# Performance work log

Measured on AMD Instinct MI355X. Metric: run time of the kernel, lower is better.

## Reference

```python
import jax, jax.numpy as jnp
import numpy as np

D_MODEL = 1024
N_HEADS = 16
D_HEAD = D_MODEL // N_HEADS


def setup_inputs() -> dict:
    key = jax.random.key(0)
    k1, k2, k3 = jax.random.split(key, 3)
    B, T = 4, 2048
    x = jax.random.normal(k1, (B, T, D_MODEL), dtype=jnp.float32)
    # torch Linear(d, 3d, bias=False): y = x @ W.T ; we store W already transposed -> [d, 3d]
    w_qkv = jax.random.normal(k2, (D_MODEL, 3 * D_MODEL), dtype=jnp.float32) * (D_MODEL ** -0.5)
    w_proj = jax.random.normal(k3, (D_MODEL, D_MODEL), dtype=jnp.float32) * (D_MODEL ** -0.5)
    return {"x": x, "w_qkv": w_qkv, "w_proj": w_proj}


def reference(x, w_qkv, w_proj):
    B, T, C = x.shape
    H, Dh = N_HEADS, D_HEAD
    qkv = (x @ w_qkv).reshape(B, T, 3, H, Dh)
    q = jnp.transpose(qkv[:, :, 0], (0, 2, 1, 3))  # [B,H,T,Dh]
    k = jnp.transpose(qkv[:, :, 1], (0, 2, 1, 3))
    v = jnp.transpose(qkv[:, :, 2], (0, 2, 1, 3))
    scale = 1.0 / jnp.sqrt(jnp.asarray(Dh, dtype=x.dtype))
    att = jnp.einsum('bhqd,bhkd->bhqk', q, k) * scale  # [B,H,T,T]
    causal = jnp.tril(jnp.ones((T, T), dtype=bool))
    att = jnp.where(causal[None, None], att, jnp.asarray(-jnp.inf, dtype=att.dtype))
    att = jax.nn.softmax(att, axis=-1)
    y = jnp.einsum('bhqk,bhkd->bhqd', att, v)          # [B,H,T,Dh]
    y = jnp.transpose(y, (0, 2, 1, 3)).reshape(B, T, C)
    return y @ w_proj
```

## Files before the change

### kernel.cpp

```cpp
#include <hip/hip_runtime.h>
#include <hip/hip_bf16.h>
#include <cmath>

#define T_SEQ 2048
#define NHEADS 16
#define DHEAD 64
#define DMODEL 1024
#define CQKV 3072

typedef __attribute__((ext_vector_type(8))) short short8;
typedef __attribute__((ext_vector_type(8))) __bf16 bf16x8;
typedef __attribute__((ext_vector_type(4))) float floatx4;

#define LDS_CAST(p) ((__attribute__((address_space(3))) void*)(p))
#define GLB_CAST(p) ((const __attribute__((address_space(1))) void*)(p))

static __device__ __forceinline__ floatx4 mfma_bf16(short8 a, short8 b, floatx4 c) {
  return __builtin_amdgcn_mfma_f32_16x16x32_bf16(
      __builtin_bit_cast(bf16x8, a), __builtin_bit_cast(bf16x8, b), c, 0, 0, 0);
}

static __device__ __forceinline__ short f2bf(float f) {
  union { float f; unsigned u; } x; x.f = f;
  unsigned r = x.u + 0x7FFFu + ((x.u >> 16) & 1u);
  return (short)(r >> 16);
}

static __device__ __forceinline__ float bf2f(short s) {
  return __builtin_bit_cast(float, ((unsigned)(unsigned short)s) << 16);
}

static __device__ __forceinline__ float exp2_(float x) {
#if __has_builtin(__builtin_amdgcn_exp2f)
  return __builtin_amdgcn_exp2f(x);
#else
  return exp2f(x);
#endif
}

static __device__ __forceinline__ bool sniff_is_bf16(const unsigned* __restrict__ x) {
  int cnt = 0;
#pragma unroll
  for (int i = 0; i < 32; ++i) {
    unsigned e = (x[i] >> 7) & 0xFFu;
    cnt += (e >= 0x70u && e <= 0x8Fu) ? 1 : 0;
  }
  return cnt >= 16;
}

static __device__ __forceinline__ short8 load8f32(const char* p, size_t idx) {
  const float4* f = (const float4*)(p + idx * 4);
  float4 a = f[0], b = f[1];
  short8 r;
  r[0] = f2bf(a.x); r[1] = f2bf(a.y); r[2] = f2bf(a.z); r[3] = f2bf(a.w);
  r[4] = f2bf(b.x); r[5] = f2bf(b.y); r[6] = f2bf(b.z); r[7] = f2bf(b.w);
  return r;
}

__global__ __launch_bounds__(256) void prep(const char* __restrict__ x,
                                            short* __restrict__ xbf,
                                            const char* __restrict__ wqkv,
                                            short* __restrict__ wqkvT,
                                            const char* __restrict__ wproj,
                                            short* __restrict__ wprojT,
                                            const unsigned* __restrict__ xs) {
  const bool isbf = sniff_is_bf16(xs);
  const int bid = blockIdx.x;
  if (bid < 4096) {
    const int i = (bid * 256 + threadIdx.x) * 8;
    if (isbf) *(short8*)(xbf + i) = *(const short8*)((const short*)x + i);
    else      *(short8*)(xbf + i) = load8f32(x, (size_t)i);
    return;
  }
  __shared__ short tile[32][33];
  const char* w; short* wt; int N, bid2;
  if (bid < 4096 + 3072) { w = wqkv;  wt = wqkvT;  N = 3072; bid2 = bid - 4096; }
  else                   { w = wproj; wt = wprojT; N = 1024; bid2 = bid - 7168; }
  const int K = 1024;
  const int ntiles = N >> 5;
  const int n0 = (bid2 % ntiles) * 32, k0 = (bid2 / ntiles) * 32;
  const int tx = threadIdx.x & 31, ty = threadIdx.x >> 5;
#pragma unroll
  for (int i = 0; i < 4; ++i) {
    const int r = ty * 4 + i;
    const size_t off = (size_t)(k0 + r) * N + n0 + tx;
    tile[r][tx] = isbf ? ((const short*)w)[off] : f2bf(((const float*)w)[off]);
  }
  __syncthreads();
#pragma unroll
  for (int i = 0; i < 4; ++i) {
    const int r = ty * 4 + i;
    wt[(size_t)(n0 + r) * K + k0 + tx] = tile[tx][r];
  }
}

__global__ __launch_bounds__(256) void gemm128(const short* __restrict__ A,
                                               const short* __restrict__ Bt,
                                               void* __restrict__ C,
                                               short* __restrict__ C2,
                                               int M, int N, int K, int mode,
                                               const unsigned* __restrict__ xs) {
  const bool out_f32 = (mode == 1) ? !sniff_is_bf16(xs) : false;

  __shared__ short as[128 * 64];
  __shared__ short bs[128 * 64];
  const int tid = threadIdx.x;
  const int wid = tid >> 6, lane = tid & 63;
  const int quad = lane >> 4, l16 = lane & 15;
  const int wm = wid >> 1, wn = wid & 1;
  const int m0 = blockIdx.y * 128, n0 = blockIdx.x * 128;

  const int srl = lane >> 3;
  const int sch = ((lane & 7) ^ srl) * 8;

  const floatx4 zero4 = {0.f, 0.f, 0.f, 0.f};
  floatx4 acc[4][4];
#pragma unroll
  for (int i = 0; i < 4; ++i)
#pragma unroll
    for (int j = 0; j < 4; ++j) acc[i][j] = zero4;

  for (int kt = 0; kt < K; kt += 64) {
    __syncthreads();
#pragma unroll
    for (int i = 0; i < 4; ++i) {
      const int row = wid * 32 + i * 8;
      const short* ga = A + (size_t)(m0 + row + srl) * K + kt + sch;
      const short* gb = Bt + (size_t)(n0 + row + srl) * K + kt + sch;
      __builtin_amdgcn_global_load_lds(GLB_CAST(ga), LDS_CAST(as + row * 64), 16, 0, 0);
      __builtin_amdgcn_global_load_lds(GLB_CAST(gb), LDS_CAST(bs + row * 64), 16, 0, 0);
    }
    __syncthreads();

#pragma unroll
    for (int kc = 0; kc < 2; ++kc) {
      const int slot = ((kc * 4 + quad) ^ (l16 & 7)) * 8;
      short8 afr[4], bfr[4];
#pragma unroll
      for (int mt = 0; mt < 4; ++mt)
        afr[mt] = *(const short8*)&as[(wm * 64 + mt * 16 + l16) * 64 + slot];
#pragma unroll
      for (int nt = 0; nt < 4; ++nt)
        bfr[nt] = *(const short8*)&bs[(wn * 64 + nt * 16 + l16) * 64 + slot];
#pragma unroll
      for (int mt = 0; mt < 4; ++mt)
#pragma unroll
        for (int nt = 0; nt < 4; ++nt)
          acc[mt][nt] = mfma_bf16(afr[mt], bfr[nt], acc[mt][nt]);
    }
  }

  const int row0 = m0 + wm * 64 + quad * 4;
  const int col0 = n0 + wn * 64 + l16;
  if (mode == 2 && n0 >= 2048) {
#pragma unroll
    for (int mt = 0; mt < 4; ++mt)
#pragma unroll
      for (int nt = 0; nt < 4; ++nt)
#pragma unroll
        for (int r = 0; r < 4; ++r) {
          const int row = row0 + mt * 16 + r;
          const int col = col0 + nt * 16;
          const int d = col & 63, hh = (col >> 6) - 32;
          const int bb = row >> 11, t = row & 2047;
          C2[((size_t)(bb * 16 + hh) * 64 + d) * T_SEQ + t] = f2bf(acc[mt][nt][r]);
        }
  } else {
    const int outN = (mode == 2) ? 2048 : N;
#pragma unroll
    for (int mt = 0; mt < 4; ++mt)
#pragma unroll
      for (int nt = 0; nt < 4; ++nt)
#pragma unroll
        for (int r = 0; r < 4; ++r) {
          const size_t off = (size_t)(row0 + mt * 16 + r) * outN + col0 + nt * 16;
          if (out_f32) ((float*)C)[off] = acc[mt][nt][r];
          else         ((short*)C)[off] = f2bf(acc[mt][nt][r]);
        }
  }
}

__global__ __launch_bounds__(512) void attn(const short* __restrict__ qk,
                                            const short* __restrict__ vT,
                                            short* __restrict__ y) {
  __shared__ short ks[2][64 * 64];
  __shared__ short vs[2][64 * 64];
  __shared__ short ps[8][16][72];
  const int tid = threadIdx.x;
  const int wid = tid >> 6, lane = tid & 63;
  const int quad = lane >> 4, l16 = lane & 15;
  const int b = blockIdx.x >> 4, h = blockIdx.x & 15;
  const int q0 = ((int)gridDim.y - 1 - (int)blockIdx.y) * 128;
  const int qw0 = q0 + wid * 16;

  const short* qbase = qk + (size_t)b * T_SEQ * 2048 + h * DHEAD;
  const short* kbase = qbase + DMODEL;
  const short* vtb = vT + (size_t)(b * NHEADS + h) * DHEAD * T_SEQ;
  const float SC = 0.18033688011112042f;

  const int srl = lane >> 3;
  const int sch = ((lane & 7) ^ srl) * 8;

  short8 aq[2];
#pragma unroll
  for (int kc = 0; kc < 2; ++kc) {
    short8 raw = *(const short8*)(qbase + (size_t)(qw0 + l16) * 2048 + kc * 32 + quad * 8);
#pragma unroll
    for (int j = 0; j < 8; ++j) aq[kc][j] = f2bf(bf2f(raw[j]) * SC);
  }

  const floatx4 zero4 = {0.f, 0.f, 0.f, 0.f};
  floatx4 o[4], lacc = zero4;
#pragma unroll
  for (int i = 0; i < 4; ++i) o[i] = zero4;
  const short8 ones8 = {0x3F80, 0x3F80, 0x3F80, 0x3F80, 0x3F80, 0x3F80, 0x3F80, 0x3F80};

  const int kend = q0 + 128;

  {
    const int row = wid * 8 + srl;
    const short* gk = kbase + (size_t)row * 2048 + sch;
    const short* gv = vtb + (size_t)row * T_SEQ + sch;
    __builtin_amdgcn_global_load_lds(GLB_CAST(gk), LDS_CAST(&ks[0][(wid * 8) * 64]), 16, 0, 0);
    __builtin_amdgcn_global_load_lds(GLB_CAST(gv), LDS_CAST(&vs[0][(wid * 8) * 64]), 16, 0, 0);
  }

  int cur = 0;
  for (int kt = 0; kt < kend; kt += 64, cur ^= 1) {
    __syncthreads();

    {
      const int ktn = (kt + 64 < kend) ? kt + 64 : kt;
      const int nxt = cur ^ 1;
      const int row = wid * 8 + srl;
      const short* gk = kbase + (size_t)(ktn + row) * 2048 + sch;
      const short* gv = vtb + (size_t)row * T_SEQ + ktn + sch;
      __builtin_amdgcn_global_load_lds(GLB_CAST(gk), LDS_CAST(&ks[nxt][(wid * 8) * 64]), 16, 0, 0);
      __builtin_amdgcn_global_load_lds(GLB_CAST(gv), LDS_CAST(&vs[nxt][(wid * 8) * 64]), 16, 0, 0);
    }

    if (kt <= qw0 + 15) {
      const short* ksc = &ks[cur][0];
      const short* vsc = &vs[cur][0];

      floatx4 s[4];
#pragma unroll
      for (int nt = 0; nt < 4; ++nt) {
        s[nt] = zero4;
#pragma unroll
        for (int kc = 0; kc < 2; ++kc) {
          const int slot = ((kc * 4 + quad) ^ (l16 & 7)) * 8;
          const short8 bk = *(const short8*)&ksc[(nt * 16 + l16) * 64 + slot];
          s[nt] = mfma_bf16(aq[kc], bk, s[nt]);
        }
      }

      const bool full = (kt + 63 <= qw0);
#pragma unroll
      for (int nt = 0; nt < 4; ++nt)
#pragma unroll
        for (int r = 0; r < 4; ++r) {
          float p = exp2_(s[nt][r]);
          if (!full) {
            const int key = kt + nt * 16 + l16;
            const int q = qw0 + quad * 4 + r;
            p = (key <= q) ? p : 0.f;
          }
          s[nt][r] = p;
        }

#pragma unroll
      for (int nt = 0; nt < 4; ++nt)
#pragma unroll
        for (int r = 0; r < 4; ++r)
          ps[wid][quad * 4 + r][nt * 16 + l16] = f2bf(s[nt][r]);

#pragma unroll
      for (int kc = 0; kc < 2; ++kc) {
        const short8 ap = *(const short8*)&ps[wid][l16][kc * 32 + quad * 8];
        lacc = mfma_bf16(ap, ones8, lacc);
#pragma unroll
        for (int d4 = 0; d4 < 4; ++d4) {
          const int slot = ((kc * 4 + quad) ^ (l16 & 7)) * 8;
          const short8 bv = *(const short8*)&vsc[(d4 * 16 + l16) * 64 + slot];
          o[d4] = mfma_bf16(ap, bv, o[d4]);
        }
      }
    }
  }

  floatx4 inv;
#pragma unroll
  for (int r = 0; r < 4; ++r) inv[r] = 1.0f / lacc[r];
#pragma unroll
  for (int d4 = 0; d4 < 4; ++d4)
#pragma unroll
    for (int r = 0; r < 4; ++r) {
      const int q = qw0 + quad * 4 + r;
      y[(size_t)(b * T_SEQ + q) * DMODEL + h * DHEAD + d4 * 16 + l16] =
          f2bf(o[d4][r] * inv[r]);
    }
}

extern "C" void kernel_launch(void* const* d_in, const int* in_sizes, int n_in,
                              void* d_out, int out_size, void* d_ws, size_t ws_size,
                              hipStream_t stream) {
  const char* x = (const char*)d_in[0];
  const char* w_qkv = (const char*)d_in[1];
  const char* w_proj = (const char*)d_in[2];
  const unsigned* xs = (const unsigned*)d_in[0];

  short* qk = (short*)d_ws;
  short* vTb = qk + (size_t)8192 * 2048;
  short* wqkvT = vTb + (size_t)64 * 64 * 2048;
  short* wprojT = wqkvT + (size_t)3072 * 1024;
  short* xbf = wprojT + (size_t)1024 * 1024;
  short* ybuf = xbf;

  prep<<<4096 + 3072 + 1024, 256, 0, stream>>>(x, xbf, w_qkv, wqkvT, w_proj, wprojT, xs);
  {
    dim3 grid(3072 / 128, 8192 / 128);
    gemm128<<<grid, 256, 0, stream>>>(xbf, wqkvT, qk, vTb, 8192, 3072, 1024, 2, xs);
  }
  {
    dim3 grid(4 * NHEADS, T_SEQ / 128);
    attn<<<grid, 512, 0, stream>>>(qk, vTb, ybuf);
  }
  {
    dim3 grid(1024 / 128, 8192 / 128);
    gemm128<<<grid, 256, 0, stream>>>(ybuf, wprojT, d_out, nullptr, 8192, 1024, 1024, 1, xs);
  }
}
```

Before: 255.3 us.

## Double-buffer GEMM LDS tiles with K-step 32 and prefetch next tile

```diff
diff --git a/kernel.cpp b/kernel.cpp
--- a/kernel.cpp
+++ b/kernel.cpp
@@ -102,16 +102,21 @@
                                                const unsigned* __restrict__ xs) {
   const bool out_f32 = (mode == 1) ? !sniff_is_bf16(xs) : false;
 
-  __shared__ short as[128 * 64];
-  __shared__ short bs[128 * 64];
+  __shared__ short as[2][128 * 32];
+  __shared__ short bs[2][128 * 32];
   const int tid = threadIdx.x;
   const int wid = tid >> 6, lane = tid & 63;
   const int quad = lane >> 4, l16 = lane & 15;
   const int wm = wid >> 1, wn = wid & 1;
   const int m0 = blockIdx.y * 128, n0 = blockIdx.x * 128;
 
-  const int srl = lane >> 3;
-  const int sch = ((lane & 7) ^ srl) * 8;
+  const int cL = tid >> 3, cs = tid & 7;
+  const int cu = cs ^ (cL & 7);
+  const int crow = 2 * cL + (cu >> 2);
+  const int ckc8 = (cu & 3) * 8;
+
+  const int lm = l16 >> 1;
+  const int slotA = ((((l16 & 1) << 2) | quad) ^ lm) * 8;
 
   const floatx4 zero4 = {0.f, 0.f, 0.f, 0.f};
   floatx4 acc[4][4];
@@ -120,35 +125,41 @@
 #pragma unroll
     for (int j = 0; j < 4; ++j) acc[i][j] = zero4;
 
-  for (int kt = 0; kt < K; kt += 64) {
+  const short* a0 = A + (size_t)(m0 + crow) * K + ckc8;
+  const short* a1 = A + (size_t)(m0 + crow + 64) * K + ckc8;
+  const short* b0 = Bt + (size_t)(n0 + crow) * K + ckc8;
+  const short* b1 = Bt + (size_t)(n0 + crow + 64) * K + ckc8;
+
+#define STG(kt_, bb)                                                              \
+  do {                                                                            \
+    __builtin_amdgcn_global_load_lds(GLB_CAST(a0 + (kt_)), LDS_CAST(&as[(bb)][wid * 512]), 16, 0, 0);        \
+    __builtin_amdgcn_global_load_lds(GLB_CAST(a1 + (kt_)), LDS_CAST(&as[(bb)][2048 + wid * 512]), 16, 0, 0); \
+    __builtin_amdgcn_global_load_lds(GLB_CAST(b0 + (kt_)), LDS_CAST(&bs[(bb)][wid * 512]), 16, 0, 0);        \
+    __builtin_amdgcn_global_load_lds(GLB_CAST(b1 + (kt_)), LDS_CAST(&bs[(bb)][2048 + wid * 512]), 16, 0, 0); \
+  } while (0)
+
+  STG(0, 0);
+
+  int cur = 0;
+  for (int kt = 0; kt < K; kt += 32, cur ^= 1) {
     __syncthreads();
-#pragma unroll
-    for (int i = 0; i < 4; ++i) {
-      const int row = wid * 32 + i * 8;
-      const short* ga = A + (size_t)(m0 + row + srl) * K + kt + sch;
-      const short* gb = Bt + (size_t)(n0 + row + srl) * K + kt + sch;
-      __builtin_amdgcn_global_load_lds(GLB_CAST(ga), LDS_CAST(as + row * 64), 16, 0, 0);
-      __builtin_amdgcn_global_load_lds(GLB_CAST(gb), LDS_CAST(bs + row * 64), 16, 0, 0);
-    }
-    __syncthreads();
-
-#pragma unroll
-    for (int kc = 0; kc < 2; ++kc) {
-      const int slot = ((kc * 4 + quad) ^ (l16 & 7)) * 8;
-      short8 afr[4], bfr[4];
-#pragma unroll
-      for (int mt = 0; mt < 4; ++mt)
-        afr[mt] = *(const short8*)&as[(wm * 64 + mt * 16 + l16) * 64 + slot];
-#pragma unroll
-      for (int nt = 0; nt < 4; ++nt)
-        bfr[nt] = *(const short8*)&bs[(wn * 64 + nt * 16 + l16) * 64 + slot];
-#pragma unroll
-      for (int mt = 0; mt < 4; ++mt)
-#pragma unroll
-        for (int nt = 0; nt < 4; ++nt)
-          acc[mt][nt] = mfma_bf16(afr[mt], bfr[nt], acc[mt][nt]);
-    }
-  }
+    const int ktn = (kt + 32 < K) ? kt + 32 : kt;
+    STG(ktn, cur ^ 1);
+
+    short8 afr[4], bfr[4];
+#pragma unroll
+    for (int mt = 0; mt < 4; ++mt)
+      afr[mt] = *(const short8*)&as[cur][(wm * 32 + mt * 8 + lm) * 64 + slotA];
+#pragma unroll
+    for (int nt = 0; nt < 4; ++nt)
+      bfr[nt] = *(const short8*)&bs[cur][(wn * 32 + nt * 8 + lm) * 64 + slotA];
+#pragma unroll
+    for (int mt = 0; mt < 4; ++mt)
+#pragma unroll
+      for (int nt = 0; nt < 4; ++nt)
+        acc[mt][nt] = mfma_bf16(afr[mt], bfr[nt], acc[mt][nt]);
+  }
+#undef STG
 
   const int row0 = m0 + wm * 64 + quad * 4;
   const int col0 = n0 + wn * 64 + l16;
```

After: 272.9 us. 1.07x slower.
